# Kernel tuning notes

Measured on AMD Instinct MI355X. Metric: run time of the kernel, lower is better.

Reference implementation:

```python
import jax, jax.numpy as jnp
import numpy as np

NUM_CAPSULE = 32
DIM_CAPSULE = 16
NUM_ITERATIONS = 3


def squash(v):
    # v: [B, O, F]; squash along last dim
    norm = jnp.linalg.norm(v, axis=-1, keepdims=True)
    mag = norm * norm
    return v / norm * mag / (1.0 + mag)


def setup_inputs() -> dict:
    key = jax.random.key(0)
    k1, k2 = jax.random.split(key)
    B, L, H = 128, 512, 256
    O, F = NUM_CAPSULE, DIM_CAPSULE
    x = jax.random.normal(k1, (B, L, H), dtype=jnp.float32)
    # xavier_normal for [1, H, O*F]: std = sqrt(2 / (H + O*F))
    std = float(np.sqrt(2.0 / (H + O * F)))
    W = jax.random.normal(k2, (1, H, O * F), dtype=jnp.float32) * std
    return {"x": x, "W": W}


def reference(x, W):
    B, I, H = x.shape
    O, F = NUM_CAPSULE, DIM_CAPSULE
    # u: [B, I, O*F] -> [B, O, I, F]
    u = jnp.matmul(x, W)  # broadcasts shared W [1,H,O*F]
    u = u.reshape(B, I, O, F).transpose(0, 2, 1, 3)
    b = jnp.zeros((B, O, I), dtype=u.dtype)
    v = None
    for _ in range(NUM_ITERATIONS):
        c = jax.nn.softmax(b, axis=1)            # softmax over output capsules O
        v = jnp.einsum('boi,boif->bof', c, u)    # weighted aggregation
        v = squash(v)
        b = jnp.einsum('bof,boif->boi', v, u)    # agreement logits
    return v
```

## Files before the change

kernel.cpp:

```cpp
#include <hip/hip_runtime.h>

#define BB 128
#define II 512
#define HH 256
#define OO 32
#define FF 16
#define OF 512
#define CI 64
#define NP 8
#define XTSTR 260
#define CSTR 72

typedef __attribute__((ext_vector_type(8))) short short8;
typedef __attribute__((ext_vector_type(4))) float floatx4;

__device__ __forceinline__ ushort f2bf(float f) {
  unsigned u = __float_as_uint(f);
  u += 0x7FFFu + ((u >> 16) & 1u);
  return (ushort)(u >> 16);
}
__device__ __forceinline__ float bf2f(ushort u) {
  return __uint_as_float(((unsigned)u) << 16);
}

__global__ __launch_bounds__(256) void k_prep(
    const float* __restrict__ x, ushort* __restrict__ x16,
    ushort* __restrict__ xT16, float* __restrict__ xsum_part) {
  __shared__ ushort xt[CI * XTSTR];
  __shared__ float4 red[4][64];
  int t = threadIdx.x;
  int blk = blockIdx.x;
  int c4 = t & 63, grp = t >> 6;
  const float* xg = x + (size_t)blk * CI * HH;
  ushort* x16g = x16 + (size_t)blk * CI * HH;
  float4 sum = make_float4(0.f, 0.f, 0.f, 0.f);
#pragma unroll
  for (int j = 0; j < 16; ++j) {
    int row = j * 4 + grp;
    float4 v4 = *(const float4*)(xg + (size_t)row * HH + c4 * 4);
    sum.x += v4.x; sum.y += v4.y; sum.z += v4.z; sum.w += v4.w;
    ushort4 u;
    u.x = f2bf(v4.x); u.y = f2bf(v4.y); u.z = f2bf(v4.z); u.w = f2bf(v4.w);
    *(ushort4*)&xt[row * XTSTR + c4 * 4] = u;
    *(ushort4*)&x16g[(size_t)row * HH + c4 * 4] = u;
  }
  red[grp][c4] = sum;
  __syncthreads();
  if (t < 64) {
    float4 s = red[0][t];
    float4 s1 = red[1][t], s2 = red[2][t], s3 = red[3][t];
    s.x += s1.x + s2.x + s3.x; s.y += s1.y + s2.y + s3.y;
    s.z += s1.z + s2.z + s3.z; s.w += s1.w + s2.w + s3.w;
    *(float4*)&xsum_part[(size_t)blk * HH + t * 4] = s;
  }
  ushort* xtg = xT16 + (size_t)blk * HH * CI + (size_t)t * CI;
#pragma unroll
  for (int ch = 0; ch < 8; ++ch) {
    ushort4 a, bq;
    a.x = xt[(ch * 8 + 0) * XTSTR + t]; a.y = xt[(ch * 8 + 1) * XTSTR + t];
    a.z = xt[(ch * 8 + 2) * XTSTR + t]; a.w = xt[(ch * 8 + 3) * XTSTR + t];
    bq.x = xt[(ch * 8 + 4) * XTSTR + t]; bq.y = xt[(ch * 8 + 5) * XTSTR + t];
    bq.z = xt[(ch * 8 + 6) * XTSTR + t]; bq.w = xt[(ch * 8 + 7) * XTSTR + t];
    *(ushort4*)(xtg + ch * 8) = a;
    *(ushort4*)(xtg + ch * 8 + 4) = bq;
  }
}

__global__ __launch_bounds__(256) void k_v1(
    const float* __restrict__ xsum_part, const float* __restrict__ W,
    ushort* __restrict__ wvT16) {
  __shared__ float cxs[HH];
  __shared__ float red[4][16];
  __shared__ float vres[FF];
  int t = threadIdx.x;
  int blk = blockIdx.x;
  int b = blk >> 5, o = blk & 31;
  {
    const float* cp = xsum_part + (size_t)b * NP * HH + t;
    float a = 0.f;
#pragma unroll
    for (int p = 0; p < NP; ++p) a += cp[(size_t)p * HH];
    cxs[t] = a * (1.0f / 32.0f);
  }
  __syncthreads();
  int f = t & 15, hq = t >> 4;
  const float* wp = W + (size_t)hq * 16 * OF + o * FF + f;
  float acc = 0.f;
#pragma unroll
  for (int j = 0; j < 16; ++j)
    acc += cxs[hq * 16 + j] * wp[(size_t)j * OF];
  acc += __shfl_xor(acc, 16);
  acc += __shfl_xor(acc, 32);
  if ((t & 63) < 16) red[t >> 6][f] = acc;
  __syncthreads();
  if (t < 16) {
    float a = red[0][t] + red[1][t] + red[2][t] + red[3][t];
    float n2 = a * a;
#pragma unroll
    for (int mask = 1; mask < 16; mask <<= 1) n2 += __shfl_xor(n2, mask);
    float scale = sqrtf(n2) / (1.f + n2);
    vres[t] = a * scale;
  }
  __syncthreads();
  const float4* wq = (const float4*)(W + (size_t)t * OF + o * FF);
  const float4* vp = (const float4*)vres;
  float a = 0.f;
#pragma unroll
  for (int q = 0; q < 4; ++q) {
    float4 w4 = wq[q], v4 = vp[q];
    a += w4.x * v4.x + w4.y * v4.y + w4.z * v4.z + w4.w * v4.w;
  }
  wvT16[((size_t)b * OO + o) * HH + t] = f2bf(a);
}

__global__ __launch_bounds__(256, 4) void k_route(
    const ushort* __restrict__ x16, const ushort* __restrict__ xT16,
    const ushort* __restrict__ wvT16, ushort* __restrict__ cxp16) {
  __shared__ ushort c2[OO * CSTR];
  int t = threadIdx.x;
  int blk = blockIdx.x;
  int b = blk >> 3;
  int lane = t & 63, w = t >> 6;
  int l16 = lane & 15, quad = lane >> 4;

  const ushort* xrow = x16 + ((size_t)blk * CI + w * 16 + l16) * HH + quad * 8;
  const ushort* wv0 = wvT16 + ((size_t)b * OO + l16) * HH + quad * 8;
  const ushort* wv1 = wv0 + 16 * HH;
  floatx4 acc0 = {0.f, 0.f, 0.f, 0.f}, acc1 = {0.f, 0.f, 0.f, 0.f};
#pragma unroll
  for (int ks = 0; ks < 8; ++ks) {
    short8 af = *(const short8*)(xrow + ks * 32);
    short8 b0 = *(const short8*)(wv0 + ks * 32);
    short8 b1 = *(const short8*)(wv1 + ks * 32);
    acc0 = __builtin_amdgcn_mfma_f32_16x16x32_bf16(af, b0, acc0, 0, 0, 0);
    acc1 = __builtin_amdgcn_mfma_f32_16x16x32_bf16(af, b1, acc1, 0, 0, 0);
  }
#pragma unroll
  for (int r = 0; r < 4; ++r) {
    float a0 = acc0[r], a1 = acc1[r];
    float m = fmaxf(a0, a1);
#pragma unroll
    for (int mask = 1; mask < 16; mask <<= 1) m = fmaxf(m, __shfl_xor(m, mask));
    float e0 = __expf(a0 - m), e1 = __expf(a1 - m);
    float s = e0 + e1;
#pragma unroll
    for (int mask = 1; mask < 16; mask <<= 1) s += __shfl_xor(s, mask);
    float inv = 1.f / s;
    int il = w * 16 + quad * 4 + r;
    c2[l16 * CSTR + il] = f2bf(e0 * inv);
    c2[(16 + l16) * CSTR + il] = f2bf(e1 * inv);
  }
  __syncthreads();

  short8 caf[2][2];
#pragma unroll
  for (int mt = 0; mt < 2; ++mt)
#pragma unroll
    for (int ks = 0; ks < 2; ++ks)
      caf[mt][ks] = *(const short8*)&c2[(mt * 16 + l16) * CSTR + ks * 32 + quad * 8];
  const ushort* xtp = xT16 + (size_t)blk * HH * CI;
  ushort* outp0 = cxp16 + (size_t)blk * OO * HH;
#pragma unroll
  for (int hi = 0; hi < 4; ++hi) {
    int ht = w * 4 + hi;
    const ushort* xtr = xtp + (size_t)(ht * 16 + l16) * CI + quad * 8;
    floatx4 d0 = {0.f, 0.f, 0.f, 0.f}, d1 = {0.f, 0.f, 0.f, 0.f};
#pragma unroll
    for (int ks = 0; ks < 2; ++ks) {
      short8 bf = *(const short8*)(xtr + ks * 32);
      d0 = __builtin_amdgcn_mfma_f32_16x16x32_bf16(caf[0][ks], bf, d0, 0, 0, 0);
      d1 = __builtin_amdgcn_mfma_f32_16x16x32_bf16(caf[1][ks], bf, d1, 0, 0, 0);
    }
    ushort* outp = outp0 + ht * 16 + l16;
#pragma unroll
    for (int r = 0; r < 4; ++r) {
      outp[(size_t)(quad * 4 + r) * HH] = f2bf(d0[r]);
      outp[(size_t)(16 + quad * 4 + r) * HH] = f2bf(d1[r]);
    }
  }
}

__global__ __launch_bounds__(256) void k_v2(
    const ushort* __restrict__ cxp16, const float* __restrict__ W,
    ushort* __restrict__ wvT16, float* __restrict__ out, int final_) {
  __shared__ float cxs[HH];
  __shared__ float red[4][16];
  __shared__ float vres[FF];
  int t = threadIdx.x;
  int blk = blockIdx.x;
  int b = blk >> 5, o = blk & 31;
  {
    const ushort* cp = cxp16 + (((size_t)b * NP) * OO + o) * HH + t;
    float a = 0.f;
#pragma unroll
    for (int p = 0; p < NP; ++p) a += bf2f(cp[(size_t)p * OO * HH]);
    cxs[t] = a;
  }
  __syncthreads();
  int f = t & 15, hq = t >> 4;
  const float* wp = W + (size_t)hq * 16 * OF + o * FF + f;
  float acc = 0.f;
#pragma unroll
  for (int j = 0; j < 16; ++j)
    acc += cxs[hq * 16 + j] * wp[(size_t)j * OF];
  acc += __shfl_xor(acc, 16);
  acc += __shfl_xor(acc, 32);
  if ((t & 63) < 16) red[t >> 6][f] = acc;
  __syncthreads();
  if (t < 16) {
    float a = red[0][t] + red[1][t] + red[2][t] + red[3][t];
    float n2 = a * a;
#pragma unroll
    for (int mask = 1; mask < 16; mask <<= 1) n2 += __shfl_xor(n2, mask);
    float scale = sqrtf(n2) / (1.f + n2);
    float res = a * scale;
    if (final_) out[(size_t)blk * FF + t] = res;
    else vres[t] = res;
  }
  if (!final_) {
    __syncthreads();
    const float4* wq = (const float4*)(W + (size_t)t * OF + o * FF);
    const float4* vp = (const float4*)vres;
    float a = 0.f;
#pragma unroll
    for (int q = 0; q < 4; ++q) {
      float4 w4 = wq[q], v4 = vp[q];
      a += w4.x * v4.x + w4.y * v4.y + w4.z * v4.z + w4.w * v4.w;
    }
    wvT16[((size_t)b * OO + o) * HH + t] = f2bf(a);
  }
}

extern "C" void kernel_launch(void* const* d_in, const int* in_sizes, int n_in,
                              void* d_out, int out_size, void* d_ws, size_t ws_size,
                              hipStream_t stream) {
  const float* x = (const float*)d_in[0];
  const float* W = (const float*)d_in[1];
  float* out = (float*)d_out;
  float* ws = (float*)d_ws;
  float*  xsum_part = ws;
  ushort* wvT16 = (ushort*)(ws + 262144);
  ushort* x16   = (ushort*)(ws + 786432);
  ushort* xT16  = (ushort*)(ws + 9175040);
  ushort* cxp16 = (ushort*)(ws + 17563648);

  k_prep<<<BB * NP, 256, 0, stream>>>(x, x16, xT16, xsum_part);
  k_v1<<<BB * OO, 256, 0, stream>>>(xsum_part, W, wvT16);
  for (int it = 0; it < 2; ++it) {
    k_route<<<BB * NP, 256, 0, stream>>>(x16, xT16, wvT16, cxp16);
    k_v2<<<BB * OO, 256, 0, stream>>>(cxp16, W, wvT16, out, it == 1);
  }
}
```

Baseline: 182.2 us.

## Drop transposed x copy; stage swizzled x tile in LDS via direct global-to-LDS loads

The prep kernel no longer writes a transposed bf16 copy of x. It writes only the row-major bf16 copy, with columns XOR-swizzled per row. Each routing block loads its 64x256 tile into LDS with global_load_lds and reads it row-wise for the first MFMA and column-wise (gathering 8 scalars) for the second. This removes one 16MB-ish write plus the repeated global reads of xT16. In exchange it uses 32KB of LDS per block, which may limit occupancy, and the scalar-gather LDS reads may be slow.

```diff
diff --git a/kernel.cpp b/kernel.cpp
--- a/kernel.cpp
+++ b/kernel.cpp
@@ -8,7 +8,6 @@
 #define OF 512
 #define CI 64
 #define NP 8
-#define XTSTR 260
 #define CSTR 72
 
 typedef __attribute__((ext_vector_type(8))) short short8;
@@ -22,17 +21,20 @@
 __device__ __forceinline__ float bf2f(ushort u) {
   return __uint_as_float(((unsigned)u) << 16);
 }
+__device__ __forceinline__ int swzrow(int i) {
+  return (i & 7) ^ (((i >> 3) & 3) << 1);
+}
 
 __global__ __launch_bounds__(256) void k_prep(
     const float* __restrict__ x, ushort* __restrict__ x16,
-    ushort* __restrict__ xT16, float* __restrict__ xsum_part) {
-  __shared__ ushort xt[CI * XTSTR];
+    float* __restrict__ xsum_part) {
   __shared__ float4 red[4][64];
   int t = threadIdx.x;
   int blk = blockIdx.x;
   int c4 = t & 63, grp = t >> 6;
   const float* xg = x + (size_t)blk * CI * HH;
   ushort* x16g = x16 + (size_t)blk * CI * HH;
+  int g = c4 >> 1, s4 = (c4 & 1) * 4;
   float4 sum = make_float4(0.f, 0.f, 0.f, 0.f);
 #pragma unroll
   for (int j = 0; j < 16; ++j) {
@@ -41,8 +43,7 @@
     sum.x += v4.x; sum.y += v4.y; sum.z += v4.z; sum.w += v4.w;
     ushort4 u;
     u.x = f2bf(v4.x); u.y = f2bf(v4.y); u.z = f2bf(v4.z); u.w = f2bf(v4.w);
-    *(ushort4*)&xt[row * XTSTR + c4 * 4] = u;
-    *(ushort4*)&x16g[(size_t)row * HH + c4 * 4] = u;
+    *(ushort4*)&x16g[row * HH + (((g ^ swzrow(row)) << 3) + s4)] = u;
   }
   red[grp][c4] = sum;
   __syncthreads();
@@ -53,17 +54,6 @@
     s.z += s1.z + s2.z + s3.z; s.w += s1.w + s2.w + s3.w;
     *(float4*)&xsum_part[(size_t)blk * HH + t * 4] = s;
   }
-  ushort* xtg = xT16 + (size_t)blk * HH * CI + (size_t)t * CI;
-#pragma unroll
-  for (int ch = 0; ch < 8; ++ch) {
-    ushort4 a, bq;
-    a.x = xt[(ch * 8 + 0) * XTSTR + t]; a.y = xt[(ch * 8 + 1) * XTSTR + t];
-    a.z = xt[(ch * 8 + 2) * XTSTR + t]; a.w = xt[(ch * 8 + 3) * XTSTR + t];
-    bq.x = xt[(ch * 8 + 4) * XTSTR + t]; bq.y = xt[(ch * 8 + 5) * XTSTR + t];
-    bq.z = xt[(ch * 8 + 6) * XTSTR + t]; bq.w = xt[(ch * 8 + 7) * XTSTR + t];
-    *(ushort4*)(xtg + ch * 8) = a;
-    *(ushort4*)(xtg + ch * 8 + 4) = bq;
-  }
 }
 
 __global__ __launch_bounds__(256) void k_v1(
@@ -114,22 +104,36 @@
 }
 
 __global__ __launch_bounds__(256, 4) void k_route(
-    const ushort* __restrict__ x16, const ushort* __restrict__ xT16,
-    const ushort* __restrict__ wvT16, ushort* __restrict__ cxp16) {
-  __shared__ ushort c2[OO * CSTR];
+    const ushort* __restrict__ x16, const ushort* __restrict__ wvT16,
+    ushort* __restrict__ cxp16) {
+  __shared__ alignas(16) ushort xs[CI * HH];
+  __shared__ alignas(16) ushort c2[OO * CSTR];
   int t = threadIdx.x;
   int blk = blockIdx.x;
   int b = blk >> 3;
   int lane = t & 63, w = t >> 6;
   int l16 = lane & 15, quad = lane >> 4;
 
-  const ushort* xrow = x16 + ((size_t)blk * CI + w * 16 + l16) * HH + quad * 8;
+  const ushort* gt = x16 + (size_t)blk * (CI * HH);
+#pragma unroll
+  for (int it = 0; it < 8; ++it) {
+    int off = (it * 4 + w) * 512;
+    __builtin_amdgcn_global_load_lds(
+        (const __attribute__((address_space(1))) unsigned*)(gt + off + lane * 8),
+        (__attribute__((address_space(3))) unsigned*)(&xs[off]), 16, 0, 0);
+  }
+  asm volatile("s_waitcnt vmcnt(0)" ::: "memory");
+  __syncthreads();
+
+  int i_a = w * 16 + l16;
+  int swa = swzrow(i_a);
+  const ushort* xrow = &xs[i_a * HH];
   const ushort* wv0 = wvT16 + ((size_t)b * OO + l16) * HH + quad * 8;
   const ushort* wv1 = wv0 + 16 * HH;
   floatx4 acc0 = {0.f, 0.f, 0.f, 0.f}, acc1 = {0.f, 0.f, 0.f, 0.f};
 #pragma unroll
   for (int ks = 0; ks < 8; ++ks) {
-    short8 af = *(const short8*)(xrow + ks * 32);
+    short8 af = *(const short8*)(xrow + (((ks * 4 + quad) ^ swa) << 3));
     short8 b0 = *(const short8*)(wv0 + ks * 32);
     short8 b1 = *(const short8*)(wv1 + ks * 32);
     acc0 = __builtin_amdgcn_mfma_f32_16x16x32_bf16(af, b0, acc0, 0, 0, 0);
@@ -158,16 +162,21 @@
 #pragma unroll
     for (int ks = 0; ks < 2; ++ks)
       caf[mt][ks] = *(const short8*)&c2[(mt * 16 + l16) * CSTR + ks * 32 + quad * 8];
-  const ushort* xtp = xT16 + (size_t)blk * HH * CI;
   ushort* outp0 = cxp16 + (size_t)blk * OO * HH;
 #pragma unroll
   for (int hi = 0; hi < 4; ++hi) {
     int ht = w * 4 + hi;
-    const ushort* xtr = xtp + (size_t)(ht * 16 + l16) * CI + quad * 8;
+    int hh = ht * 16 + l16;
+    int gq = hh >> 3, sub = hh & 7;
     floatx4 d0 = {0.f, 0.f, 0.f, 0.f}, d1 = {0.f, 0.f, 0.f, 0.f};
 #pragma unroll
     for (int ks = 0; ks < 2; ++ks) {
-      short8 bf = *(const short8*)(xtr + ks * 32);
+      short8 bf;
+#pragma unroll
+      for (int e = 0; e < 8; ++e) {
+        int i = ks * 32 + quad * 8 + e;
+        bf[e] = (short)xs[i * HH + (((gq ^ e ^ (quad << 1)) << 3) + sub)];
+      }
       d0 = __builtin_amdgcn_mfma_f32_16x16x32_bf16(caf[0][ks], bf, d0, 0, 0, 0);
       d1 = __builtin_amdgcn_mfma_f32_16x16x32_bf16(caf[1][ks], bf, d1, 0, 0, 0);
     }
@@ -241,13 +250,12 @@
   float*  xsum_part = ws;
   ushort* wvT16 = (ushort*)(ws + 262144);
   ushort* x16   = (ushort*)(ws + 786432);
-  ushort* xT16  = (ushort*)(ws + 9175040);
-  ushort* cxp16 = (ushort*)(ws + 17563648);
-
-  k_prep<<<BB * NP, 256, 0, stream>>>(x, x16, xT16, xsum_part);
+  ushort* cxp16 = (ushort*)(ws + 9175040);
+
+  k_prep<<<BB * NP, 256, 0, stream>>>(x, x16, xsum_part);
   k_v1<<<BB * OO, 256, 0, stream>>>(xsum_part, W, wvT16);
   for (int it = 0; it < 2; ++it) {
-    k_route<<<BB * NP, 256, 0, stream>>>(x16, xT16, wvT16, cxp16);
+    k_route<<<BB * NP, 256, 0, stream>>>(x16, wvT16, cxp16);
     k_v2<<<BB * OO, 256, 0, stream>>>(cxp16, W, wvT16, out, it == 1);
   }
 }
```

New measurement: 166.8 us. 8.4% less time.
